# Kernel optimization log

Measured on AMD Instinct MI355X. Metric: run time of the kernel, lower is better.

The kernel has to match this reference:

```python
import jax, jax.numpy as jnp
import numpy as np

BN_EPS = 1e-5


def _gin_layer(x, src, dst, W, b, num_nodes):
    # GINConv with eps=0: h_i = MLP(x_i + sum_{j in N(i)} x_j)
    agg = jax.ops.segment_sum(x[src], dst, num_segments=num_nodes)  # [N, F]
    h = (x + agg) @ W + b
    return jax.nn.relu(h)


def _batchnorm(h, gamma, beta):
    # training-mode BatchNorm1d: biased batch stats over the node dim
    mean = jnp.mean(h, axis=0)
    var = jnp.mean(jnp.square(h - mean), axis=0)
    return (h - mean) * jax.lax.rsqrt(var + BN_EPS) * gamma + beta


def setup_inputs() -> dict:
    key = jax.random.key(0)
    N, E, F, H = 50000, 800000, 128, 128
    ks = jax.random.split(key, 6)
    x = jax.random.normal(ks[0], (N, F), dtype=jnp.float32)
    edge_index = jax.random.randint(ks[1], (2, E), 0, N, dtype=jnp.int64)
    W1 = jax.random.normal(ks[2], (F, H), dtype=jnp.float32) * 0.05
    b1 = jnp.zeros((H,), dtype=jnp.float32)
    W2 = jax.random.normal(ks[3], (H, H), dtype=jnp.float32) * 0.05
    b2 = jnp.zeros((H,), dtype=jnp.float32)
    g1 = jnp.ones((H,), dtype=jnp.float32)
    be1 = jnp.zeros((H,), dtype=jnp.float32)
    g2 = jnp.ones((H,), dtype=jnp.float32)
    be2 = jnp.zeros((H,), dtype=jnp.float32)
    return {"x": x, "edge_index": edge_index, "W1": W1, "b1": b1,
            "W2": W2, "b2": b2, "g1": g1, "be1": be1, "g2": g2, "be2": be2}


def reference(x, edge_index, W1, b1, W2, b2, g1, be1, g2, be2):
    N = x.shape[0]
    src, dst = edge_index[0], edge_index[1]
    h = _gin_layer(x, src, dst, W1, b1, N)
    h = _batchnorm(h, g1, be1)
    h = _gin_layer(h, src, dst, W2, b2, N)
    return _batchnorm(h, g2, be2)
```

## Files before the change

kernel.cpp:

```cpp
#include <hip/hip_runtime.h>
#include <hip/hip_fp16.h>

#define FDIM 128
#define NGRP 8
#define CAP  64

typedef _Float16 half8_t __attribute__((ext_vector_type(8)));
typedef _Float16 half4_t __attribute__((ext_vector_type(4)));
typedef float float4_t __attribute__((ext_vector_type(4)));


__global__ void prep_kernel(int* __restrict__ zbase, int zn,
                            const float* __restrict__ x, _Float16* __restrict__ xh, int n4x,
                            const float* __restrict__ W1, _Float16* __restrict__ Wf1,
                            const float* __restrict__ W2, _Float16* __restrict__ Wf2,
                            int nzb, int ncb) {
  int b = blockIdx.x, t = threadIdx.x;
  if (b < nzb) {
    int i = b * 256 + t;
    if (i < zn) zbase[i] = 0;
  } else if (b < nzb + ncb) {
    int i = (b - nzb) * 256 + t;
    if (i < n4x) {
      float4 v = ((const float4*)x)[i];
      half4_t h;
      h.x = (_Float16)v.x; h.y = (_Float16)v.y; h.z = (_Float16)v.z; h.w = (_Float16)v.w;
      ((half4_t*)xh)[i] = h;
    }
  } else {
    int gid = (b - nzb - ncb) * 256 + t;
    int which = gid >> 14;
    int tid = gid & 16383;
    const float* W = which ? W2 : W1;
    _Float16* Wf = which ? Wf2 : Wf1;
    int j = tid & 7, lane = (tid >> 3) & 63, rest = tid >> 9;
    int kb = rest & 3, ct = (rest >> 2) & 1, wave = rest >> 3;
    int quad = lane >> 4, m16 = lane & 15;
    int k = kb * 32 + quad * 8 + j;
    int n = wave * 32 + ct * 16 + m16;
    Wf[tid] = (_Float16)W[k * FDIM + n];
  }
}


__global__ void place_part_kernel(const int* __restrict__ src, const int* __restrict__ dst,
                                  int* __restrict__ deg, int* __restrict__ ssrc,
                                  int E, int step) {
  int grp = blockIdx.x & (NGRP - 1);
  int nb = gridDim.x >> 3, bid = blockIdx.x >> 3;
  int lo = grp * step, hi = lo + step;
  int E4 = E >> 2;
  const int4* d4 = (const int4*)dst;
  const int4* s4 = (const int4*)src;
  for (int i = bid * blockDim.x + threadIdx.x; i < E4; i += nb * blockDim.x) {
    int4 d = d4[i];
    bool m0 = d.x >= lo && d.x < hi, m1 = d.y >= lo && d.y < hi;
    bool m2 = d.z >= lo && d.z < hi, m3 = d.w >= lo && d.w < hi;
    if (m0 | m1 | m2 | m3) {
      int4 s = s4[i];
      if (m0) { int p = atomicAdd(&deg[d.x], 1); if (p < CAP) ssrc[(d.x << 6) + p] = s.x; }
      if (m1) { int p = atomicAdd(&deg[d.y], 1); if (p < CAP) ssrc[(d.y << 6) + p] = s.y; }
      if (m2) { int p = atomicAdd(&deg[d.z], 1); if (p < CAP) ssrc[(d.z << 6) + p] = s.z; }
      if (m3) { int p = atomicAdd(&deg[d.w], 1); if (p < CAP) ssrc[(d.w << 6) + p] = s.w; }
    }
  }
  for (int e = (E4 << 2) + bid * blockDim.x + threadIdx.x; e < E; e += nb * blockDim.x) {
    int d = dst[e];
    if (d >= lo && d < hi) {
      int p = atomicAdd(&deg[d], 1);
      if (p < CAP) ssrc[(d << 6) + p] = src[e];
    }
  }
}


__device__ inline float2 up2(unsigned u) {
  __half2 h = *(__half2*)&u;
  return __half22float2(h);
}

__device__ inline void addrow(float* a, uint4 v) {
  float2 p0 = up2(v.x), p1 = up2(v.y), p2 = up2(v.z), p3 = up2(v.w);
  a[0] += p0.x; a[1] += p0.y; a[2] += p1.x; a[3] += p1.y;
  a[4] += p2.x; a[5] += p2.y; a[6] += p3.x; a[7] += p3.y;
}

template <bool LAYER2>
__global__ __launch_bounds__(256) void fused_kernel(
    const uint4* __restrict__ x4, const int* __restrict__ deg,
    const int* __restrict__ ssrc, const float* __restrict__ ascale,
    const _Float16* __restrict__ Wf, const float* __restrict__ bias,
    const float* __restrict__ r2v, _Float16* __restrict__ outh,
    float* __restrict__ ssum, float* __restrict__ ssq,
    const float* __restrict__ gamma, const float* __restrict__ beta,
    const float* __restrict__ W2, float* __restrict__ aout, float* __restrict__ cout,
    int* __restrict__ counter, int N) {
  int t = threadIdx.x;
  int wave = t >> 6, lane = t & 63;
  int quad = lane >> 4, m16 = lane & 15;
  int row0 = blockIdx.x * 64;

  __shared__ __align__(16) unsigned char sAb[64 * 256];
  __shared__ float sdn[64];
  __shared__ float scc[FDIM];
  __shared__ int isLast;

  if (LAYER2 && t < 64) {
    int r = row0 + t;
    sdn[t] = (r < N) ? (float)(deg[r] + 1) : 0.f;
  }

  if (row0 + 64 > N) {
    for (int j = t; j < 64 * 16; j += 256) ((uint4*)sAb)[j] = make_uint4(0u, 0u, 0u, 0u);
    __syncthreads();
  }

  for (int i = 0; i < 16; i++) {
    int ln = wave * 16 + i;
    int node = row0 + ln;
    if (node >= N) break;
    int d = deg[node];
    if (d > CAP) d = CAP;
    int idx = ssrc[(node << 6) + lane];

    float a0[8], a1[8];
    {
      uint4 v = x4[(size_t)node * 16 + m16];
      float w0 = (quad == 0) ? 1.f : 0.f;
      float2 p0 = up2(v.x), p1 = up2(v.y), p2 = up2(v.z), p3 = up2(v.w);
      a0[0] = p0.x * w0; a0[1] = p0.y * w0; a0[2] = p1.x * w0; a0[3] = p1.y * w0;
      a0[4] = p2.x * w0; a0[5] = p2.y * w0; a0[6] = p3.x * w0; a0[7] = p3.y * w0;
#pragma unroll
      for (int j = 0; j < 8; j++) a1[j] = 0.f;
    }

    int d4 = d >> 2, tail = d & 3;
    int g = 0;
    for (; g + 3 < d4; g += 4) {
      int s0 = __shfl(idx, 4 * g + quad);
      int s1 = __shfl(idx, 4 * g + 4 + quad);
      int s2 = __shfl(idx, 4 * g + 8 + quad);
      int s3 = __shfl(idx, 4 * g + 12 + quad);
      uint4 v0 = x4[(size_t)s0 * 16 + m16];
      uint4 v1 = x4[(size_t)s1 * 16 + m16];
      uint4 v2 = x4[(size_t)s2 * 16 + m16];
      uint4 v3 = x4[(size_t)s3 * 16 + m16];
      addrow(a0, v0); addrow(a1, v1); addrow(a0, v2); addrow(a1, v3);
    }
    for (; g + 1 < d4; g += 2) {
      int s0 = __shfl(idx, 4 * g + quad);
      int s1 = __shfl(idx, 4 * g + 4 + quad);
      uint4 v0 = x4[(size_t)s0 * 16 + m16];
      uint4 v1 = x4[(size_t)s1 * 16 + m16];
      addrow(a0, v0); addrow(a1, v1);
    }
    if (g < d4) {
      int s0 = __shfl(idx, 4 * g + quad);
      uint4 v0 = x4[(size_t)s0 * 16 + m16];
      addrow(a0, v0);
    }
    if (tail) {
      int pos = 4 * d4 + quad;
      int s = __shfl(idx, pos);
      bool ok = quad < tail;
      int ss = ok ? s : node;
      uint4 v = x4[(size_t)ss * 16 + m16];
      float w = ok ? 1.f : 0.f;
      float2 p0 = up2(v.x), p1 = up2(v.y), p2 = up2(v.z), p3 = up2(v.w);
      a1[0] += p0.x * w; a1[1] += p0.y * w; a1[2] += p1.x * w; a1[3] += p1.y * w;
      a1[4] += p2.x * w; a1[5] += p2.y * w; a1[6] += p3.x * w; a1[7] += p3.y * w;
    }

#pragma unroll
    for (int j = 0; j < 8; j++) a0[j] += a1[j];
#pragma unroll
    for (int j = 0; j < 8; j++) {
      a0[j] += __shfl_xor(a0[j], 16);
      a0[j] += __shfl_xor(a0[j], 32);
    }

    if (LAYER2) {
      float4 av0 = ((const float4*)ascale)[2 * m16];
      float4 av1 = ((const float4*)ascale)[2 * m16 + 1];
      a0[0] *= av0.x; a0[1] *= av0.y; a0[2] *= av0.z; a0[3] *= av0.w;
      a0[4] *= av1.x; a0[5] *= av1.y; a0[6] *= av1.z; a0[7] *= av1.w;
    }

    if (quad == 0) {
      __half2 h0 = __floats2half2_rn(a0[0], a0[1]);
      __half2 h1 = __floats2half2_rn(a0[2], a0[3]);
      __half2 h2 = __floats2half2_rn(a0[4], a0[5]);
      __half2 h3 = __floats2half2_rn(a0[6], a0[7]);
      uint4 r;
      r.x = *(unsigned*)&h0; r.y = *(unsigned*)&h1;
      r.z = *(unsigned*)&h2; r.w = *(unsigned*)&h3;
      *(uint4*)(sAb + ln * 256 + ((m16 * 16) ^ ((ln & 7) << 4))) = r;
    }
  }
  __syncthreads();

  half8_t bf[2][4];
  const half8_t* wf8 = (const half8_t*)Wf;
#pragma unroll
  for (int ct = 0; ct < 2; ct++)
#pragma unroll
    for (int kb = 0; kb < 4; kb++)
      bf[ct][kb] = wf8[(size_t)(((wave * 2 + ct) * 4 + kb) * 64 + lane)];

  float4_t acc[4][2] = {};
#pragma unroll
  for (int rt = 0; rt < 4; rt++) {
    int arow = rt * 16 + m16;
#pragma unroll
    for (int kb = 0; kb < 4; kb++) {
      half8_t av = *(const half8_t*)(sAb + arow * 256 +
                                     ((kb * 64 + quad * 16) ^ ((arow & 7) << 4)));
      acc[rt][0] = __builtin_amdgcn_mfma_f32_16x16x32_f16(av, bf[0][kb], acc[rt][0], 0, 0, 0);
      acc[rt][1] = __builtin_amdgcn_mfma_f32_16x16x32_f16(av, bf[1][kb], acc[rt][1], 0, 0, 0);
    }
  }

#pragma unroll
  for (int ct = 0; ct < 2; ct++) {
    int col = wave * 32 + ct * 16 + m16;
    float bv = bias[col];
    float rv = LAYER2 ? r2v[col] : 0.f;
    float s = 0.f, q = 0.f;
#pragma unroll
    for (int rt = 0; rt < 4; rt++) {
#pragma unroll
      for (int r = 0; r < 4; r++) {
        int row = row0 + rt * 16 + quad * 4 + r;
        if (row < N) {
          float v = acc[rt][ct][r] + bv;
          if (LAYER2) v += sdn[rt * 16 + quad * 4 + r] * rv;
          v = fmaxf(v, 0.f);
          outh[(size_t)row * FDIM + col] = (_Float16)v;
          s += v; q += v * v;
        }
      }
    }
    s += __shfl_xor(s, 16); q += __shfl_xor(q, 16);
    s += __shfl_xor(s, 32); q += __shfl_xor(q, 32);
    if (quad == 0) {
      atomicAdd(&ssum[col], s);
      atomicAdd(&ssq[col], q);
    }
  }

  __syncthreads();
  if (t == 0) {
    int v = atomicAdd(counter, 1);
    isLast = (v == (int)gridDim.x - 1);
  }
  __syncthreads();
  if (!isLast) return;

  if (t < FDIM) {
    float sm = atomicAdd(&ssum[t], 0.f);
    float qv = atomicAdd(&ssq[t], 0.f);
    float invn = 1.f / (float)N;
    float mean = sm * invn;
    float var = qv * invn - mean * mean;
    float rs = rsqrtf(var + 1e-5f);
    float av = gamma[t] * rs;
    aout[t] = av;
    float cv = beta[t] - mean * av;
    if (LAYER2) cout[t] = cv;
    else scc[t] = cv;
  }
  if (!LAYER2) {
    __syncthreads();
    if (t < FDIM) {
      float acc2 = 0.f;
      for (int k = 0; k < FDIM; k++) acc2 += scc[k] * W2[k * FDIM + t];
      cout[t] = acc2;
    }
  }
}


__global__ void apply_h_kernel(const uint2* __restrict__ h4, const float* __restrict__ a,
                               const float* __restrict__ c, float4* __restrict__ out, int n4) {
  int i = blockIdx.x * blockDim.x + threadIdx.x;
  if (i < n4) {
    uint2 u = h4[i];
    float2 v0 = up2(u.x), v1 = up2(u.y);
    int c4 = i & 31;
    float4 av = ((const float4*)a)[c4];
    float4 cv = ((const float4*)c)[c4];
    float4 o;
    o.x = av.x * v0.x + cv.x;
    o.y = av.y * v0.y + cv.y;
    o.z = av.z * v1.x + cv.z;
    o.w = av.w * v1.y + cv.w;
    out[i] = o;
  }
}


extern "C" void kernel_launch(void* const* d_in, const int* in_sizes, int n_in,
                              void* d_out, int out_size, void* d_ws, size_t ws_size,
                              hipStream_t stream) {
  const float* x   = (const float*)d_in[0];
  const int*   ei  = (const int*)d_in[1];
  const float* W1  = (const float*)d_in[2];
  const float* b1  = (const float*)d_in[3];
  const float* W2  = (const float*)d_in[4];
  const float* b2  = (const float*)d_in[5];
  const float* g1  = (const float*)d_in[6];
  const float* be1 = (const float*)d_in[7];
  const float* g2  = (const float*)d_in[8];
  const float* be2 = (const float*)d_in[9];
  float* out = (float*)d_out;

  const int N = in_sizes[0] / FDIM;
  const int E = in_sizes[1] / 2;
  const int* src = ei;
  const int* dst = ei + E;

  auto align256 = [](char*& q) { q = (char*)(((uintptr_t)q + 255) & ~(uintptr_t)255); };

  char* p = (char*)d_ws;
  int* deg = (int*)p;        p += (size_t)N * 4;
  float* stats = (float*)p;  p += 1280 * 4;
  align256(p);
  int* ssrc = (int*)p;       p += (size_t)N * CAP * 4; align256(p);
  _Float16* xh  = (_Float16*)p; p += (size_t)N * FDIM * 2; align256(p);
  _Float16* h1  = (_Float16*)p; p += (size_t)N * FDIM * 2; align256(p);
  _Float16* h2  = (_Float16*)p; p += (size_t)N * FDIM * 2; align256(p);
  _Float16* Wf1 = (_Float16*)p; p += FDIM * FDIM * 2;
  _Float16* Wf2 = (_Float16*)p; p += FDIM * FDIM * 2;

  float* s1 = stats + 0,   *q1 = stats + 128;
  float* s2 = stats + 256, *q2 = stats + 384;
  float* a1 = stats + 512, *r2 = stats + 640;
  float* a2 = stats + 768, *c2 = stats + 896;
  int* cnt1 = (int*)(stats + 1024);
  int* cnt2 = (int*)(stats + 1088);

  const int ntiles = (N + 63) / 64;
  const int step = (N + NGRP - 1) / NGRP;

  const int zn = N + 1280;
  const int nzb = (zn + 255) / 256;
  const int n4x = N * 32;
  const int ncb = (n4x + 255) / 256;

  prep_kernel<<<nzb + ncb + 128, 256, 0, stream>>>((int*)deg, zn, x, xh, n4x,
                                                   W1, Wf1, W2, Wf2, nzb, ncb);
  place_part_kernel<<<NGRP * 128, 256, 0, stream>>>(src, dst, deg, ssrc, E, step);

  fused_kernel<false><<<ntiles, 256, 0, stream>>>((const uint4*)xh, deg, ssrc, nullptr,
                                                  Wf1, b1, nullptr, h1, s1, q1,
                                                  g1, be1, W2, a1, r2, cnt1, N);

  fused_kernel<true><<<ntiles, 256, 0, stream>>>((const uint4*)h1, deg, ssrc, a1,
                                                 Wf2, b2, r2, h2, s2, q2,
                                                 g2, be2, nullptr, a2, c2, cnt2, N);

  int n4 = N * 32;
  apply_h_kernel<<<(n4 + 255) / 256, 256, 0, stream>>>((const uint2*)h2, a2, c2,
                                                       (float4*)out, n4);
}
```

Baseline: 259.8 us.

## Gather two nodes per iteration with masked loads and prefetch next pair

```diff
diff --git a/kernel.cpp b/kernel.cpp
--- a/kernel.cpp
+++ b/kernel.cpp
@@ -79,10 +79,12 @@
   return __half22float2(h);
 }
 
-__device__ inline void addrow(float* a, uint4 v) {
+__device__ inline void addroww(float* a, uint4 v, float w) {
   float2 p0 = up2(v.x), p1 = up2(v.y), p2 = up2(v.z), p3 = up2(v.w);
-  a[0] += p0.x; a[1] += p0.y; a[2] += p1.x; a[3] += p1.y;
-  a[4] += p2.x; a[5] += p2.y; a[6] += p3.x; a[7] += p3.y;
+  a[0] = fmaf(w, p0.x, a[0]); a[1] = fmaf(w, p0.y, a[1]);
+  a[2] = fmaf(w, p1.x, a[2]); a[3] = fmaf(w, p1.y, a[3]);
+  a[4] = fmaf(w, p2.x, a[4]); a[5] = fmaf(w, p2.y, a[5]);
+  a[6] = fmaf(w, p3.x, a[6]); a[7] = fmaf(w, p3.y, a[7]);
 }
 
 template <bool LAYER2>
@@ -115,86 +117,127 @@
     __syncthreads();
   }
 
-  for (int i = 0; i < 16; i++) {
-    int ln = wave * 16 + i;
-    int node = row0 + ln;
-    if (node >= N) break;
-    int d = deg[node];
-    if (d > CAP) d = CAP;
-    int idx = ssrc[(node << 6) + lane];
-
-    float a0[8], a1[8];
-    {
-      uint4 v = x4[(size_t)node * 16 + m16];
-      float w0 = (quad == 0) ? 1.f : 0.f;
-      float2 p0 = up2(v.x), p1 = up2(v.y), p2 = up2(v.z), p3 = up2(v.w);
-      a0[0] = p0.x * w0; a0[1] = p0.y * w0; a0[2] = p1.x * w0; a0[3] = p1.y * w0;
-      a0[4] = p2.x * w0; a0[5] = p2.y * w0; a0[6] = p3.x * w0; a0[7] = p3.y * w0;
-#pragma unroll
-      for (int j = 0; j < 8; j++) a1[j] = 0.f;
-    }
-
-    int d4 = d >> 2, tail = d & 3;
-    int g = 0;
-    for (; g + 3 < d4; g += 4) {
-      int s0 = __shfl(idx, 4 * g + quad);
-      int s1 = __shfl(idx, 4 * g + 4 + quad);
-      int s2 = __shfl(idx, 4 * g + 8 + quad);
-      int s3 = __shfl(idx, 4 * g + 12 + quad);
-      uint4 v0 = x4[(size_t)s0 * 16 + m16];
-      uint4 v1 = x4[(size_t)s1 * 16 + m16];
-      uint4 v2 = x4[(size_t)s2 * 16 + m16];
-      uint4 v3 = x4[(size_t)s3 * 16 + m16];
-      addrow(a0, v0); addrow(a1, v1); addrow(a0, v2); addrow(a1, v3);
-    }
-    for (; g + 1 < d4; g += 2) {
-      int s0 = __shfl(idx, 4 * g + quad);
-      int s1 = __shfl(idx, 4 * g + 4 + quad);
-      uint4 v0 = x4[(size_t)s0 * 16 + m16];
-      uint4 v1 = x4[(size_t)s1 * 16 + m16];
-      addrow(a0, v0); addrow(a1, v1);
-    }
-    if (g < d4) {
-      int s0 = __shfl(idx, 4 * g + quad);
-      uint4 v0 = x4[(size_t)s0 * 16 + m16];
-      addrow(a0, v0);
-    }
-    if (tail) {
-      int pos = 4 * d4 + quad;
-      int s = __shfl(idx, pos);
-      bool ok = quad < tail;
-      int ss = ok ? s : node;
-      uint4 v = x4[(size_t)ss * 16 + m16];
-      float w = ok ? 1.f : 0.f;
-      float2 p0 = up2(v.x), p1 = up2(v.y), p2 = up2(v.z), p3 = up2(v.w);
-      a1[0] += p0.x * w; a1[1] += p0.y * w; a1[2] += p1.x * w; a1[3] += p1.y * w;
-      a1[4] += p2.x * w; a1[5] += p2.y * w; a1[6] += p3.x * w; a1[7] += p3.y * w;
-    }
-
-#pragma unroll
-    for (int j = 0; j < 8; j++) a0[j] += a1[j];
-#pragma unroll
-    for (int j = 0; j < 8; j++) {
-      a0[j] += __shfl_xor(a0[j], 16);
-      a0[j] += __shfl_xor(a0[j], 32);
-    }
-
-    if (LAYER2) {
-      float4 av0 = ((const float4*)ascale)[2 * m16];
-      float4 av1 = ((const float4*)ascale)[2 * m16 + 1];
-      a0[0] *= av0.x; a0[1] *= av0.y; a0[2] *= av0.z; a0[3] *= av0.w;
-      a0[4] *= av1.x; a0[5] *= av1.y; a0[6] *= av1.z; a0[7] *= av1.w;
-    }
-
-    if (quad == 0) {
-      __half2 h0 = __floats2half2_rn(a0[0], a0[1]);
-      __half2 h1 = __floats2half2_rn(a0[2], a0[3]);
-      __half2 h2 = __floats2half2_rn(a0[4], a0[5]);
-      __half2 h3 = __floats2half2_rn(a0[6], a0[7]);
-      uint4 r;
-      r.x = *(unsigned*)&h0; r.y = *(unsigned*)&h1;
-      r.z = *(unsigned*)&h2; r.w = *(unsigned*)&h3;
-      *(uint4*)(sAb + ln * 256 + ((m16 * 16) ^ ((ln & 7) << 4))) = r;
+  {
+    int base = row0 + wave * 16;
+    int dAp = 0, dBp = 0, idxAp = 0, idxBp = 0;
+    uint4 selfAp = make_uint4(0u, 0u, 0u, 0u), selfBp = selfAp;
+    if (base < N) {
+      dAp = deg[base];
+      idxAp = ssrc[(base << 6) + lane];
+      selfAp = x4[(size_t)base * 16 + m16];
+    }
+    if (base + 1 < N) {
+      dBp = deg[base + 1];
+      idxBp = ssrc[((base + 1) << 6) + lane];
+      selfBp = x4[(size_t)(base + 1) * 16 + m16];
+    }
+    for (int ip = 0; ip < 8; ip++) {
+      int curA = base + 2 * ip;
+      if (curA >= N) break;
+      int curB = curA + 1;
+      bool vB = curB < N;
+      int dA = dAp, dB = dBp;
+      int idxA = idxAp, idxB = idxBp;
+      uint4 selfA = selfAp, selfB = selfBp;
+      if (dA > CAP) dA = CAP;
+      if (dB > CAP) dB = CAP;
+      if (!vB) dB = 0;
+
+      int nxA = curA + 2, nxB = curA + 3;
+      if (ip + 1 < 8) {
+        if (nxA < N) {
+          dAp = deg[nxA];
+          idxAp = ssrc[(nxA << 6) + lane];
+          selfAp = x4[(size_t)nxA * 16 + m16];
+        }
+        if (nxB < N) {
+          dBp = deg[nxB];
+          idxBp = ssrc[(nxB << 6) + lane];
+          selfBp = x4[(size_t)nxB * 16 + m16];
+        }
+      }
+
+      float aA0[8], aA1[8], aB0[8], aB1[8];
+      {
+        float wsA = (quad == 0) ? 1.f : 0.f;
+        float wsB = (quad == 0 && vB) ? 1.f : 0.f;
+        float2 p0 = up2(selfA.x), p1 = up2(selfA.y), p2 = up2(selfA.z), p3 = up2(selfA.w);
+        aA0[0] = p0.x * wsA; aA0[1] = p0.y * wsA; aA0[2] = p1.x * wsA; aA0[3] = p1.y * wsA;
+        aA0[4] = p2.x * wsA; aA0[5] = p2.y * wsA; aA0[6] = p3.x * wsA; aA0[7] = p3.y * wsA;
+        float2 q0 = up2(selfB.x), q1 = up2(selfB.y), q2 = up2(selfB.z), q3 = up2(selfB.w);
+        aB0[0] = q0.x * wsB; aB0[1] = q0.y * wsB; aB0[2] = q1.x * wsB; aB0[3] = q1.y * wsB;
+        aB0[4] = q2.x * wsB; aB0[5] = q2.y * wsB; aB0[6] = q3.x * wsB; aB0[7] = q3.y * wsB;
+#pragma unroll
+        for (int j = 0; j < 8; j++) { aA1[j] = 0.f; aB1[j] = 0.f; }
+      }
+
+      int dmax = dA > dB ? dA : dB;
+      int nb = (dmax + 15) >> 4;
+      for (int b = 0; b < nb; b++) {
+        int p = 16 * b + quad;
+        int sA0 = __shfl(idxA, p),      sA1 = __shfl(idxA, p + 4);
+        int sA2 = __shfl(idxA, p + 8),  sA3 = __shfl(idxA, p + 12);
+        int sB0 = __shfl(idxB, p),      sB1 = __shfl(idxB, p + 4);
+        int sB2 = __shfl(idxB, p + 8),  sB3 = __shfl(idxB, p + 12);
+        float wA0 = (p < dA) ? 1.f : 0.f,      wA1 = (p + 4 < dA) ? 1.f : 0.f;
+        float wA2 = (p + 8 < dA) ? 1.f : 0.f,  wA3 = (p + 12 < dA) ? 1.f : 0.f;
+        float wB0 = (p < dB) ? 1.f : 0.f,      wB1 = (p + 4 < dB) ? 1.f : 0.f;
+        float wB2 = (p + 8 < dB) ? 1.f : 0.f,  wB3 = (p + 12 < dB) ? 1.f : 0.f;
+        int cA0 = (p < dA) ? sA0 : curA,       cA1 = (p + 4 < dA) ? sA1 : curA;
+        int cA2 = (p + 8 < dA) ? sA2 : curA,   cA3 = (p + 12 < dA) ? sA3 : curA;
+        int cB0 = (p < dB) ? sB0 : curA,       cB1 = (p + 4 < dB) ? sB1 : curA;
+        int cB2 = (p + 8 < dB) ? sB2 : curA,   cB3 = (p + 12 < dB) ? sB3 : curA;
+        uint4 vA0 = x4[(size_t)cA0 * 16 + m16], vA1 = x4[(size_t)cA1 * 16 + m16];
+        uint4 vA2 = x4[(size_t)cA2 * 16 + m16], vA3 = x4[(size_t)cA3 * 16 + m16];
+        uint4 vB0 = x4[(size_t)cB0 * 16 + m16], vB1 = x4[(size_t)cB1 * 16 + m16];
+        uint4 vB2 = x4[(size_t)cB2 * 16 + m16], vB3 = x4[(size_t)cB3 * 16 + m16];
+        addroww(aA0, vA0, wA0); addroww(aA1, vA1, wA1);
+        addroww(aA0, vA2, wA2); addroww(aA1, vA3, wA3);
+        addroww(aB0, vB0, wB0); addroww(aB1, vB1, wB1);
+        addroww(aB0, vB2, wB2); addroww(aB1, vB3, wB3);
+      }
+
+#pragma unroll
+      for (int j = 0; j < 8; j++) { aA0[j] += aA1[j]; aB0[j] += aB1[j]; }
+#pragma unroll
+      for (int j = 0; j < 8; j++) {
+        aA0[j] += __shfl_xor(aA0[j], 16);
+        aA0[j] += __shfl_xor(aA0[j], 32);
+        aB0[j] += __shfl_xor(aB0[j], 16);
+        aB0[j] += __shfl_xor(aB0[j], 32);
+      }
+
+      if (LAYER2) {
+        float4 av0 = ((const float4*)ascale)[2 * m16];
+        float4 av1 = ((const float4*)ascale)[2 * m16 + 1];
+        aA0[0] *= av0.x; aA0[1] *= av0.y; aA0[2] *= av0.z; aA0[3] *= av0.w;
+        aA0[4] *= av1.x; aA0[5] *= av1.y; aA0[6] *= av1.z; aA0[7] *= av1.w;
+        aB0[0] *= av0.x; aB0[1] *= av0.y; aB0[2] *= av0.z; aB0[3] *= av0.w;
+        aB0[4] *= av1.x; aB0[5] *= av1.y; aB0[6] *= av1.z; aB0[7] *= av1.w;
+      }
+
+      if (quad == 0) {
+        int lnA = wave * 16 + 2 * ip;
+        __half2 h0 = __floats2half2_rn(aA0[0], aA0[1]);
+        __half2 h1 = __floats2half2_rn(aA0[2], aA0[3]);
+        __half2 h2 = __floats2half2_rn(aA0[4], aA0[5]);
+        __half2 h3 = __floats2half2_rn(aA0[6], aA0[7]);
+        uint4 r;
+        r.x = *(unsigned*)&h0; r.y = *(unsigned*)&h1;
+        r.z = *(unsigned*)&h2; r.w = *(unsigned*)&h3;
+        *(uint4*)(sAb + lnA * 256 + ((m16 * 16) ^ ((lnA & 7) << 4))) = r;
+        if (vB) {
+          int lnB = lnA + 1;
+          __half2 g0 = __floats2half2_rn(aB0[0], aB0[1]);
+          __half2 g1 = __floats2half2_rn(aB0[2], aB0[3]);
+          __half2 g2 = __floats2half2_rn(aB0[4], aB0[5]);
+          __half2 g3 = __floats2half2_rn(aB0[6], aB0[7]);
+          uint4 rb;
+          rb.x = *(unsigned*)&g0; rb.y = *(unsigned*)&g1;
+          rb.z = *(unsigned*)&g2; rb.w = *(unsigned*)&g3;
+          *(uint4*)(sAb + lnB * 256 + ((m16 * 16) ^ ((lnB & 7) << 4))) = rb;
+        }
+      }
     }
   }
   __syncthreads();
```

Result: slower. 268.6 us (+3.4%).
